# Performance work log

Hardware: AMD Instinct MI355X
Metric: run time of the kernel (lower is better)

## Reference

```python
import jax, jax.numpy as jnp
import numpy as np

# DMP constants (from DMPNet defaults)
N = 5            # number of RBF basis functions
DOF = 7          # len(state_index)
T = 10
L = 10           # subsample stride l
TAU = 1.0
A_Z = 15.0
A_X = 1.0
SCALE = 1.0      # args.scale (external CLI constant)
DT = TAU / (T * L)                      # 0.01
TIME_STEPS = int(round(TAU / DT)) + 1   # 101
BATCH = 65536
OUT_DIM = N * DOF + DOF                 # 42


def _dmp_integrate(output, y0, dy0):
    # output: [B, DOF*(N+1)]  (goal | weights), y0/dy0: [B*DOF]
    c = jnp.exp(-A_X * jnp.linspace(0.0, 1.0, N)).astype(jnp.float32)      # [N]
    sigma2 = (jnp.float32(N) ** 1.5) / c / A_X                              # [N]
    goal = output[:, :DOF].reshape(-1)                                      # [B*DOF]
    w = output[:, DOF:DOF * (N + 1)].reshape(-1, N)                         # [B*DOF, N]
    b_z = A_Z / 4.0
    z0 = dy0 * TAU

    def step(carry, _):
        x, y, z = carry
        x = x + (-A_X * x * TAU) * DT                      # canonical system
        psi = jnp.exp(-0.5 * (x - c) ** 2 / sigma2)        # [N]
        fx = (w @ psi) * x * (goal - y0) / jnp.sum(psi)    # forcing term [B*DOF]
        dz = (A_Z * (b_z * (goal - y) - z) + fx) * TAU
        dy = z * TAU
        y = y + dy * DT
        z = z + dz * DT
        return (x, y, z), y

    (_, _, _), Ys = jax.lax.scan(step, (jnp.float32(1.0), y0, z0), None, length=TIME_STEPS - 1)
    Y = jnp.concatenate([y0[None, :], Ys], axis=0)         # [TIME_STEPS, B*DOF]
    return Y.T                                              # [B*DOF, TIME_STEPS]


def setup_inputs() -> dict:
    key = jax.random.key(0)
    k1, k2, k3 = jax.random.split(key, 3)
    x = jax.random.normal(k1, (BATCH, 256), dtype=jnp.float32)       # backbone feature
    state = jax.random.normal(k2, (BATCH, DOF), dtype=jnp.float32)   # robot state
    W = jax.random.normal(k3, (256, OUT_DIM), dtype=jnp.float32) * 0.05  # fc_last weight
    b = jnp.zeros((OUT_DIM,), dtype=jnp.float32)                     # fc_last bias
    return {"x": x, "state": state, "W": W, "b": b}


def reference(x, state, W, b):
    # num_layers == 1: no hidden layers, fc_last directly on the 256-d feature
    output = (x @ W + b) * SCALE                   # [B, 42]
    y0 = state.reshape(-1)                          # [B*DOF]
    dy0 = jnp.ones_like(y0) * 0.05
    Y = _dmp_integrate(output, y0, dy0)             # [B*DOF, TIME_STEPS]
    y = Y.reshape(x.shape[0], DOF, TIME_STEPS)[:, :, ::L]   # [B, DOF, 11]
    return jnp.transpose(y, (0, 2, 1))              # [B, 11, DOF]
```

## Files before the change

### kernel.cpp

```cpp
#include <hip/hip_runtime.h>
#include <math.h>


constexpr double dexp(double z) {
    double t = z / 64.0;
    double s = 1.0, term = 1.0;
    for (int n = 1; n <= 14; ++n) { term *= t / (double)n; s += term; }
    for (int i = 0; i < 6; ++i) s *= s;
    return s;
}

struct Tbl { float v[88]; };

constexpr Tbl make_tbl() {
    Tbl T{};
    double c[5] = {}, s2[5] = {};
    for (int i = 0; i < 5; ++i) {
        c[i]  = dexp(-0.25 * (double)i);
        s2[i] = 11.180339887498949 / c[i];
    }
    double hh[101] = {}, aa[101] = {};
    double m00 = 1, m01 = 0, m10 = 0, m11 = 1;
    for (int t = 0; t <= 100; ++t) {
        hh[t] = m01; aa[t] = m00;
        const double n00 = m00 - 0.5625 * m01;
        const double n01 = 0.01 * m00 + 0.85 * m01;
        const double n10 = m10 - 0.5625 * m11;
        const double n11 = 0.01 * m10 + 0.85 * m11;
        m00 = n00; m01 = n01; m10 = n10; m11 = n11;
    }
    double vv[101][5] = {};
    double xs = 1.0;
    for (int s = 1; s <= 100; ++s) {
        xs *= 0.99;
        double psi[5] = {}, sum = 0.0;
        for (int i = 0; i < 5; ++i) {
            const double d = xs - c[i];
            psi[i] = dexp(-0.5 * d * d / s2[i]);
            sum += psi[i];
        }
        for (int i = 0; i < 5; ++i) vv[s][i] = psi[i] * xs / sum;
    }
    for (int tt = 0; tt < 11; ++tt) {
        const int T10 = 10 * tt;
        double cg = 0.0;
        for (int k = 0; k < T10; ++k) cg += hh[k];
        T.v[tt * 8 + 0] = (float)aa[T10];
        T.v[tt * 8 + 1] = (float)(0.5625 * cg);
        T.v[tt * 8 + 2] = (float)(hh[T10] * 0.05);
        for (int i = 0; i < 5; ++i) {
            double V = 0.0;
            for (int s = 1; s <= T10; ++s) V += hh[T10 - s] * vv[s][i];
            T.v[tt * 8 + 3 + i] = (float)(0.01 * V);
        }
    }
    return T;
}

constexpr Tbl TBL = make_tbl();

#define XT0 0
#define XT1 2080
#define PP  4160

__global__ __launch_bounds__(256, 4) void dmp_fused_kernel(
    const float* __restrict__ x,
    const float* __restrict__ state,
    const float* __restrict__ W,
    const float* __restrict__ bias,
    float* __restrict__ out)
{
    __shared__ float L[9620];

    const int tid  = threadIdx.x;
    const int wave = __builtin_amdgcn_readfirstlane(tid >> 6);
    const int lane = tid & 63;
    const size_t row0 = (size_t)blockIdx.x * 64;

    const int srow0 = tid >> 3;
    const int q4    = (tid & 7) * 4;
    const float* xb = x + row0 * 256;

    float4 ra, rb;

    ra = *(const float4*)(xb + (size_t)srow0 * 256 + q4);
    rb = *(const float4*)(xb + (size_t)(srow0 + 32) * 256 + q4);

    float acc[42];
#pragma unroll
    for (int ch = 0; ch < 42; ++ch) acc[ch] = 0.f;

    {
        const int b0 = XT0 + q4 * 65 + srow0;
        L[b0]            = ra.x; L[b0 + 65]       = ra.y;
        L[b0 + 130]      = ra.z; L[b0 + 195]      = ra.w;
        const int b1 = XT0 + q4 * 65 + srow0 + 32;
        L[b1]            = rb.x; L[b1 + 65]       = rb.y;
        L[b1 + 130]      = rb.z; L[b1 + 195]      = rb.w;
    }
    ra = *(const float4*)(xb + (size_t)srow0 * 256 + 32 + q4);
    rb = *(const float4*)(xb + (size_t)(srow0 + 32) * 256 + 32 + q4);
    __syncthreads();

    const int kw = wave * 8;

#pragma unroll 1
    for (int c = 0; c < 8; ++c) {
        const int cur = (c & 1) ? XT1 : XT0;
        const int nxt = (c & 1) ? XT0 : XT1;

        if (c < 7) {
            const int b0 = nxt + q4 * 65 + srow0;
            L[b0]       = ra.x; L[b0 + 65]  = ra.y;
            L[b0 + 130] = ra.z; L[b0 + 195] = ra.w;
            const int b1 = nxt + q4 * 65 + srow0 + 32;
            L[b1]       = rb.x; L[b1 + 65]  = rb.y;
            L[b1 + 130] = rb.z; L[b1 + 195] = rb.w;
        }
        if (c < 6) {
            const int ko = (c + 2) * 32 + q4;
            ra = *(const float4*)(xb + (size_t)srow0 * 256 + ko);
            rb = *(const float4*)(xb + (size_t)(srow0 + 32) * 256 + ko);
        }
        const float* Wb = W + (size_t)(c * 32 + kw) * 42;
#pragma unroll
        for (int j = 0; j < 8; ++j) {
            const float xv = L[cur + (kw + j) * 65 + lane];
#pragma unroll
            for (int ch = 0; ch < 42; ++ch)
                acc[ch] = fmaf(xv, Wb[j * 42 + ch], acc[ch]);
        }
        __syncthreads();
    }

    if (wave < 2) {
#pragma unroll
        for (int ch = 0; ch < 42; ++ch) {
            const float bv = (wave == 0) ? bias[ch] : 0.f;
            L[PP + (wave * 42 + ch) * 65 + lane] = acc[ch] + bv;
        }
    }
    __syncthreads();
    if (wave >= 2) {
#pragma unroll
        for (int ch = 0; ch < 42; ++ch) {
            const int idx = PP + ((wave - 2) * 42 + ch) * 65 + lane;
            L[idx] += acc[ch];
        }
    }
    __syncthreads();

#pragma unroll 1
    for (int pass = 0; pass < 2; ++pass) {
        if (tid < 224) {
            const int item = pass * 224 + tid;
            const int row  = item / 7;
            const int d    = item - row * 7;
            const int lrow = row - pass * 32;

            const int ch0 = d;
            const int chw = 7 + 5 * d;
            const float goal = L[PP + ch0 * 65 + row] + L[PP + (42 + ch0) * 65 + row];
            float w_[5];
#pragma unroll
            for (int i = 0; i < 5; ++i)
                w_[i] = L[PP + (chw + i) * 65 + row] + L[PP + (42 + chw + i) * 65 + row];

            const float y0 = state[row0 * 7 + item];
            const float gp = goal - y0;

#pragma unroll
            for (int tt = 0; tt < 11; ++tt) {
                float p = TBL.v[tt * 8 + 3] * w_[0];
                p = fmaf(TBL.v[tt * 8 + 4], w_[1], p);
                p = fmaf(TBL.v[tt * 8 + 5], w_[2], p);
                p = fmaf(TBL.v[tt * 8 + 6], w_[3], p);
                p = fmaf(TBL.v[tt * 8 + 7], w_[4], p);
                float y = fmaf(TBL.v[tt * 8 + 0], y0, TBL.v[tt * 8 + 2]);
                y = fmaf(TBL.v[tt * 8 + 1], goal, y);
                y = fmaf(gp, p, y);
                L[lrow * 77 + tt * 7 + d] = y;
            }
        }
        __syncthreads();
#pragma unroll
        for (int i = 0; i < 3; ++i) {
            const int idx = i * 256 + tid;
            if (idx < 616) {
                const float4 v = *(const float4*)&L[idx * 4];
                *(float4*)(out + row0 * 77 + (size_t)pass * 2464 + (size_t)idx * 4) = v;
            }
        }
        __syncthreads();
    }
}

extern "C" void kernel_launch(void* const* d_in, const int* in_sizes, int n_in,
                              void* d_out, int out_size, void* d_ws, size_t ws_size,
                              hipStream_t stream) {
    const float* x     = (const float*)d_in[0];
    const float* state = (const float*)d_in[1];
    const float* W     = (const float*)d_in[2];
    const float* b     = (const float*)d_in[3];
    float* out = (float*)d_out;

    dmp_fused_kernel<<<1024, 256, 0, stream>>>(x, state, W, b, out);
}
```

Before: 125.2 us.

## Replace scalar FMA projection with fp16 MFMA using pre-transposed weights

The 256x42 projection moves from per-thread scalar FMAs over a K-split across waves to 16x16x32 fp16 MFMA instructions. A small setup kernel converts W to a transposed, zero-padded fp16 copy in workspace each call. Each block converts its x tile to fp16 in LDS, so the cross-wave partial-sum reduction and one output pass go away. Rounding x and W to fp16 adds numerical error, and the extra single-block launch adds fixed overhead.

```diff
diff --git a/kernel.cpp b/kernel.cpp
--- a/kernel.cpp
+++ b/kernel.cpp
@@ -1,6 +1,10 @@
 #include <hip/hip_runtime.h>
 #include <math.h>
 
+
+typedef _Float16 half8 __attribute__((ext_vector_type(8)));
+typedef _Float16 half4 __attribute__((ext_vector_type(4)));
+typedef float f32x4 __attribute__((ext_vector_type(4)));
 
 constexpr double dexp(double z) {
     double t = z / 64.0;
@@ -59,139 +63,118 @@
 
 constexpr Tbl TBL = make_tbl();
 
-#define XT0 0
-#define XT1 2080
-#define PP  4160
+__global__ __launch_bounds__(256) void wt_setup_kernel(
+    const float* __restrict__ W, _Float16* __restrict__ wt)
+{
+    __shared__ float s[10752];
+    for (int f = threadIdx.x; f < 10752; f += 256) s[f] = W[f];
+    __syncthreads();
+    for (int o = threadIdx.x; o < 12288; o += 256) {
+        const int col = o >> 8, k = o & 255;
+        wt[o] = (col < 42) ? (_Float16)s[k * 42 + col] : (_Float16)0.f;
+    }
+}
 
-__global__ __launch_bounds__(256, 4) void dmp_fused_kernel(
+__global__ __launch_bounds__(256, 3) void dmp_mfma_kernel(
     const float* __restrict__ x,
     const float* __restrict__ state,
-    const float* __restrict__ W,
+    const _Float16* __restrict__ wt,
     const float* __restrict__ bias,
     float* __restrict__ out)
 {
-    __shared__ float L[9620];
+    __shared__ __align__(16) char LDS[47104];
+    _Float16* xt = (_Float16*)LDS;
+    float* P  = (float*)(LDS + 33792);
+    float* OB = (float*)LDS;
 
     const int tid  = threadIdx.x;
-    const int wave = __builtin_amdgcn_readfirstlane(tid >> 6);
+    const int wave = tid >> 6;
     const int lane = tid & 63;
+    const int n    = lane & 15;
+    const int quad = lane >> 4;
     const size_t row0 = (size_t)blockIdx.x * 64;
-
-    const int srow0 = tid >> 3;
-    const int q4    = (tid & 7) * 4;
     const float* xb = x + row0 * 256;
 
-    float4 ra, rb;
+    half8 bf[24];
+#pragma unroll
+    for (int it = 0; it < 8; ++it)
+#pragma unroll
+        for (int t = 0; t < 3; ++t)
+            bf[it * 3 + t] =
+                *(const half8*)(wt + (t * 16 + n) * 256 + it * 32 + quad * 8);
 
-    ra = *(const float4*)(xb + (size_t)srow0 * 256 + q4);
-    rb = *(const float4*)(xb + (size_t)(srow0 + 32) * 256 + q4);
-
-    float acc[42];
 #pragma unroll
-    for (int ch = 0; ch < 42; ++ch) acc[ch] = 0.f;
-
-    {
-        const int b0 = XT0 + q4 * 65 + srow0;
-        L[b0]            = ra.x; L[b0 + 65]       = ra.y;
-        L[b0 + 130]      = ra.z; L[b0 + 195]      = ra.w;
-        const int b1 = XT0 + q4 * 65 + srow0 + 32;
-        L[b1]            = rb.x; L[b1 + 65]       = rb.y;
-        L[b1 + 130]      = rb.z; L[b1 + 195]      = rb.w;
-    }
-    ra = *(const float4*)(xb + (size_t)srow0 * 256 + 32 + q4);
-    rb = *(const float4*)(xb + (size_t)(srow0 + 32) * 256 + 32 + q4);
-    __syncthreads();
-
-    const int kw = wave * 8;
-
-#pragma unroll 1
-    for (int c = 0; c < 8; ++c) {
-        const int cur = (c & 1) ? XT1 : XT0;
-        const int nxt = (c & 1) ? XT0 : XT1;
-
-        if (c < 7) {
-            const int b0 = nxt + q4 * 65 + srow0;
-            L[b0]       = ra.x; L[b0 + 65]  = ra.y;
-            L[b0 + 130] = ra.z; L[b0 + 195] = ra.w;
-            const int b1 = nxt + q4 * 65 + srow0 + 32;
-            L[b1]       = rb.x; L[b1 + 65]  = rb.y;
-            L[b1 + 130] = rb.z; L[b1 + 195] = rb.w;
-        }
-        if (c < 6) {
-            const int ko = (c + 2) * 32 + q4;
-            ra = *(const float4*)(xb + (size_t)srow0 * 256 + ko);
-            rb = *(const float4*)(xb + (size_t)(srow0 + 32) * 256 + ko);
-        }
-        const float* Wb = W + (size_t)(c * 32 + kw) * 42;
+    for (int b = 0; b < 2; ++b) {
+        float4 v[8];
 #pragma unroll
         for (int j = 0; j < 8; ++j) {
-            const float xv = L[cur + (kw + j) * 65 + lane];
+            const int f = (b * 8 + j) * 256 + tid;
+            v[j] = *(const float4*)(xb + (size_t)(f >> 6) * 256 + (f & 63) * 4);
+        }
 #pragma unroll
-            for (int ch = 0; ch < 42; ++ch)
-                acc[ch] = fmaf(xv, Wb[j * 42 + ch], acc[ch]);
-        }
-        __syncthreads();
-    }
-
-    if (wave < 2) {
-#pragma unroll
-        for (int ch = 0; ch < 42; ++ch) {
-            const float bv = (wave == 0) ? bias[ch] : 0.f;
-            L[PP + (wave * 42 + ch) * 65 + lane] = acc[ch] + bv;
-        }
-    }
-    __syncthreads();
-    if (wave >= 2) {
-#pragma unroll
-        for (int ch = 0; ch < 42; ++ch) {
-            const int idx = PP + ((wave - 2) * 42 + ch) * 65 + lane;
-            L[idx] += acc[ch];
+        for (int j = 0; j < 8; ++j) {
+            const int f = (b * 8 + j) * 256 + tid;
+            const int row = f >> 6, slot = f & 63;
+            half4 h = { (_Float16)v[j].x, (_Float16)v[j].y,
+                        (_Float16)v[j].z, (_Float16)v[j].w };
+            *(half4*)(xt + row * 264 + slot * 4) = h;
         }
     }
     __syncthreads();
 
-#pragma unroll 1
-    for (int pass = 0; pass < 2; ++pass) {
-        if (tid < 224) {
-            const int item = pass * 224 + tid;
-            const int row  = item / 7;
-            const int d    = item - row * 7;
-            const int lrow = row - pass * 32;
+    f32x4 a0 = {0.f, 0.f, 0.f, 0.f};
+    f32x4 a1 = {0.f, 0.f, 0.f, 0.f};
+    f32x4 a2 = {0.f, 0.f, 0.f, 0.f};
+    const int arow = wave * 16 + n;
+#pragma unroll
+    for (int it = 0; it < 8; ++it) {
+        const half8 a = *(const half8*)(xt + arow * 264 + it * 32 + quad * 8);
+        a0 = __builtin_amdgcn_mfma_f32_16x16x32_f16(a, bf[it * 3 + 0], a0, 0, 0, 0);
+        a1 = __builtin_amdgcn_mfma_f32_16x16x32_f16(a, bf[it * 3 + 1], a1, 0, 0, 0);
+        a2 = __builtin_amdgcn_mfma_f32_16x16x32_f16(a, bf[it * 3 + 2], a2, 0, 0, 0);
+    }
 
-            const int ch0 = d;
-            const int chw = 7 + 5 * d;
-            const float goal = L[PP + ch0 * 65 + row] + L[PP + (42 + ch0) * 65 + row];
-            float w_[5];
+    const int prow = wave * 16 + quad * 4;
 #pragma unroll
-            for (int i = 0; i < 5; ++i)
-                w_[i] = L[PP + (chw + i) * 65 + row] + L[PP + (42 + chw + i) * 65 + row];
+    for (int r = 0; r < 4; ++r) {
+        P[(prow + r) * 52 + n]      = a0[r];
+        P[(prow + r) * 52 + 16 + n] = a1[r];
+        P[(prow + r) * 52 + 32 + n] = a2[r];
+    }
+    __syncthreads();
 
-            const float y0 = state[row0 * 7 + item];
-            const float gp = goal - y0;
+    for (int item = tid; item < 448; item += 256) {
+        const int row = item / 7;
+        const int d   = item - row * 7;
+        const float goal = P[row * 52 + d] + bias[d];
+        float w_[5];
+#pragma unroll
+        for (int i = 0; i < 5; ++i)
+            w_[i] = P[row * 52 + 7 + 5 * d + i] + bias[7 + 5 * d + i];
+        const float y0 = state[row0 * 7 + item];
+        const float gp = goal - y0;
+#pragma unroll
+        for (int tt = 0; tt < 11; ++tt) {
+            float p = TBL.v[tt * 8 + 3] * w_[0];
+            p = fmaf(TBL.v[tt * 8 + 4], w_[1], p);
+            p = fmaf(TBL.v[tt * 8 + 5], w_[2], p);
+            p = fmaf(TBL.v[tt * 8 + 6], w_[3], p);
+            p = fmaf(TBL.v[tt * 8 + 7], w_[4], p);
+            float y = fmaf(TBL.v[tt * 8 + 0], y0, TBL.v[tt * 8 + 2]);
+            y = fmaf(TBL.v[tt * 8 + 1], goal, y);
+            y = fmaf(gp, p, y);
+            OB[row * 77 + tt * 7 + d] = y;
+        }
+    }
+    __syncthreads();
 
 #pragma unroll
-            for (int tt = 0; tt < 11; ++tt) {
-                float p = TBL.v[tt * 8 + 3] * w_[0];
-                p = fmaf(TBL.v[tt * 8 + 4], w_[1], p);
-                p = fmaf(TBL.v[tt * 8 + 5], w_[2], p);
-                p = fmaf(TBL.v[tt * 8 + 6], w_[3], p);
-                p = fmaf(TBL.v[tt * 8 + 7], w_[4], p);
-                float y = fmaf(TBL.v[tt * 8 + 0], y0, TBL.v[tt * 8 + 2]);
-                y = fmaf(TBL.v[tt * 8 + 1], goal, y);
-                y = fmaf(gp, p, y);
-                L[lrow * 77 + tt * 7 + d] = y;
-            }
+    for (int i = 0; i < 5; ++i) {
+        const int idx = i * 256 + tid;
+        if (idx < 1232) {
+            const float4 v = *(const float4*)(OB + idx * 4);
+            *(float4*)(out + row0 * 77 + (size_t)idx * 4) = v;
         }
-        __syncthreads();
-#pragma unroll
-        for (int i = 0; i < 3; ++i) {
-            const int idx = i * 256 + tid;
-            if (idx < 616) {
-                const float4 v = *(const float4*)&L[idx * 4];
-                *(float4*)(out + row0 * 77 + (size_t)pass * 2464 + (size_t)idx * 4) = v;
-            }
-        }
-        __syncthreads();
     }
 }
 
@@ -202,7 +185,9 @@
     const float* state = (const float*)d_in[1];
     const float* W     = (const float*)d_in[2];
     const float* b     = (const float*)d_in[3];
+    _Float16* wt = (_Float16*)d_ws;
     float* out = (float*)d_out;
 
-    dmp_fused_kernel<<<1024, 256, 0, stream>>>(x, state, W, b, out);
+    wt_setup_kernel<<<1, 256, 0, stream>>>(W, wt);
+    dmp_mfma_kernel<<<1024, 256, 0, stream>>>(x, state, wt, b, out);
 }
```

Result: faster. 113.9 us (-9.0%).
